# Performance work log

Hardware: AMD Instinct MI355X
Metric: run time of the kernel (lower is better)

Reference implementation:

```python
import jax, jax.numpy as jnp
import numpy as np

EMB = 1024
HEAD = 64

def setup_inputs() -> dict:
    key = jax.random.key(0)
    ks = jax.random.split(key, 7)
    s = 1.0 / np.sqrt(EMB)
    X = jax.random.normal(ks[0], (4, 4096, EMB), dtype=jnp.float32)
    Wk = jax.random.uniform(ks[1], (EMB, HEAD), jnp.float32, -s, s)
    bk = jax.random.uniform(ks[2], (HEAD,), jnp.float32, -s, s)
    Wq = jax.random.uniform(ks[3], (EMB, HEAD), jnp.float32, -s, s)
    bq = jax.random.uniform(ks[4], (HEAD,), jnp.float32, -s, s)
    Wv = jax.random.uniform(ks[5], (EMB, HEAD), jnp.float32, -s, s)
    bv = jax.random.uniform(ks[6], (HEAD,), jnp.float32, -s, s)
    return {"X": X, "Wk": Wk, "bk": bk, "Wq": Wq, "bq": bq, "Wv": Wv, "bv": bv}

def reference(X, Wk, bk, Wq, bq, Wv, bv):
    # X: [B, S, E]; projections -> [B, S, H]
    k = X @ Wk + bk
    q = X @ Wq + bq
    v = X @ Wv + bv
    S = X.shape[1]
    scale = 1.0 / np.sqrt(HEAD).astype(np.float32)
    scores = jnp.einsum('bqh,bkh->bqk', q, k) * scale  # [B, S, S]
    causal = jnp.tril(jnp.ones((S, S), dtype=bool))
    scores = jnp.where(causal, scores, -jnp.inf)
    probs = jax.nn.softmax(scores, axis=-1)
    return jnp.einsum('bqk,bkh->bqh', probs, v)
```

## Files before the change

### kernel.cpp

```cpp
#include <hip/hip_runtime.h>

#define S_LEN 4096
#define EMBD  1024
#define HEADD 64

typedef __bf16 bf16x8 __attribute__((ext_vector_type(8)));
typedef float  f32x4  __attribute__((ext_vector_type(4)));

__device__ __forceinline__ unsigned short f2bf(float f) {
  union { float f; unsigned u; } x; x.f = f;
  unsigned r = x.u + 0x7FFFu + ((x.u >> 16) & 1u);
  return (unsigned short)(r >> 16);
}

__device__ __forceinline__ bf16x8 cvt8(f32x4 a, f32x4 b) {
  union { bf16x8 v; unsigned short s[8]; } u;
#pragma unroll
  for (int j = 0; j < 4; j++) { u.s[j] = f2bf(a[j]); u.s[4 + j] = f2bf(b[j]); }
  return u.v;
}

__device__ __forceinline__ unsigned fbits(float f) {
  union { float f; unsigned u; } x; x.f = f; return x.u;
}

__global__ void prep_w(const float* __restrict__ Wk, const float* __restrict__ bk,
                       const float* __restrict__ Wq, const float* __restrict__ bq,
                       const float* __restrict__ Wv, const float* __restrict__ bv,
                       unsigned short* __restrict__ wt, float* __restrict__ bias) {
  int n = blockIdx.x;
  int t = threadIdx.x;
  const float QSCALE = 0.125f * 1.44269504088896340736f;
  const float* W; const float* bsrc; int col; float s = 1.0f;
  if (n < 64)       { W = Wk; bsrc = bk; col = n; }
  else if (n < 128) { W = Wq; bsrc = bq; col = n - 64; s = QSCALE; }
  else              { W = Wv; bsrc = bv; col = n - 128; }
  for (int k = t; k < EMBD; k += 256)
    wt[n * EMBD + k] = f2bf(W[k * HEADD + col] * s);
  if (t == 0) bias[n] = bsrc[col] * s;
}

__global__ __launch_bounds__(256, 1) void proj_qkv(
    const float* __restrict__ X, const unsigned short* __restrict__ wt,
    const float* __restrict__ bias,
    unsigned short* __restrict__ qws, unsigned short* __restrict__ kws,
    unsigned short* __restrict__ vtws) {
  __shared__ unsigned short xs[64 * 256];

  const int tid = threadIdx.x;
  const int w = tid >> 6;
  const int lane = tid & 63;
  const int l15 = lane & 15, lg = lane >> 4;
  const int row0 = blockIdx.x * 64;

  const int sr = tid >> 5;
  const int sc = (tid & 31) * 8;

  const unsigned short* wp = wt + (size_t)(w * 48 + l15) * EMBD + lg * 8;

  f32x4 acc[4][3];
#pragma unroll
  for (int g = 0; g < 4; g++)
#pragma unroll
    for (int j = 0; j < 3; j++) acc[g][j] = (f32x4){0.f, 0.f, 0.f, 0.f};

  f32x4 la[8], lb[8];
#pragma unroll
  for (int it = 0; it < 8; it++) {
    const float* src = X + (size_t)(row0 + it * 8 + sr) * EMBD + sc;
    la[it] = *(const f32x4*)src;
    lb[it] = *(const f32x4*)(src + 4);
  }
#pragma unroll
  for (int it = 0; it < 8; it++) {
    const int r = it * 8 + sr;
    int soff = (r << 8) + sc;
    soff ^= (r & 7) << 3;
    *(bf16x8*)&xs[soff] = cvt8(la[it], lb[it]);
  }
  __syncthreads();

#pragma unroll
  for (int kc = 0; kc < 4; kc++) {
    if (kc + 1 < 4) {
#pragma unroll
      for (int it = 0; it < 8; it++) {
        const float* src = X + (size_t)(row0 + it * 8 + sr) * EMBD + (kc + 1) * 256 + sc;
        la[it] = *(const f32x4*)src;
        lb[it] = *(const f32x4*)(src + 4);
      }
    }
    bf16x8 wf[2][3];
#pragma unroll
    for (int j = 0; j < 3; j++)
      wf[0][j] = *(const bf16x8*)(wp + (size_t)j * 16 * EMBD + kc * 256);
#pragma unroll
    for (int ss = 0; ss < 8; ss++) {
      const int cur = ss & 1;
      if (ss + 1 < 8) {
#pragma unroll
        for (int j = 0; j < 3; j++)
          wf[cur ^ 1][j] = *(const bf16x8*)(wp + (size_t)j * 16 * EMBD + kc * 256 + (ss + 1) * 32);
      }
      const int c = ss * 32 + lg * 8;
      bf16x8 a[4];
#pragma unroll
      for (int g = 0; g < 4; g++) {
        int so = ((g * 16 + l15) << 8) + c;
        so ^= (l15 & 7) << 3;
        a[g] = *(const bf16x8*)&xs[so];
      }
#pragma unroll
      for (int j = 0; j < 3; j++)
#pragma unroll
        for (int g = 0; g < 4; g++)
          acc[g][j] = __builtin_amdgcn_mfma_f32_16x16x32_bf16(a[g], wf[cur][j], acc[g][j], 0, 0, 0);
    }
    __syncthreads();
    if (kc + 1 < 4) {
#pragma unroll
      for (int it = 0; it < 8; it++) {
        const int r = it * 8 + sr;
        int soff = (r << 8) + sc;
        soff ^= (r & 7) << 3;
        *(bf16x8*)&xs[soff] = cvt8(la[it], lb[it]);
      }
      __syncthreads();
    }
  }

#pragma unroll
  for (int g = 0; g < 4; g++) {
    const int crow0 = row0 + g * 16 + lg * 4;
#pragma unroll
    for (int j = 0; j < 3; j++) {
      const int nf = w * 3 + j;
      const int n = nf * 16 + l15;
      const float bs = bias[n];
      if (nf < 8) {
        unsigned short* dst = (nf < 4) ? kws : qws;
        const int nn = n & 63;
#pragma unroll
        for (int i = 0; i < 4; i++)
          dst[(size_t)(crow0 + i) * HEADD + nn] = f2bf(acc[g][j][i] + bs);
      } else {
        const int d = n - 128;
        const int bb = crow0 >> 12, sr2 = crow0 & 4095;
        union { unsigned long long pk; unsigned short s[4]; } u;
#pragma unroll
        for (int i = 0; i < 4; i++) u.s[i] = f2bf(acc[g][j][i] + bs);
        *(unsigned long long*)&vtws[((size_t)bb * HEADD + d) * S_LEN + sr2] = u.pk;
      }
    }
  }
}

__global__ __launch_bounds__(512, 2) void attn(
    const unsigned short* __restrict__ qws,
    const unsigned short* __restrict__ kws,
    const unsigned short* __restrict__ vtws,
    unsigned short* __restrict__ pO,
    float* __restrict__ pmv, float* __restrict__ plv) {
  __shared__ uint4 kvb[2][1024];
  __shared__ unsigned short pbl[8][16][72];

  const int tid = threadIdx.x;
  const int w = tid >> 6;
  const int lane = tid & 63;
  const int l15 = lane & 15, lg = lane >> 4;
  const int srow = tid >> 3;
  const int scol = (tid & 7) * 8;
  const int soff = ((srow * 128 + (tid & 7) * 16)) ^ ((srow & 7) << 4);

  const int id = blockIdx.x;
  const int b = id & 3;
  const int x = (id >> 2) & 15;
  const int h = id >> 6;

  const unsigned short* kb = kws + (size_t)b * S_LEN * HEADD;
  const unsigned short* vb = vtws + (size_t)b * HEADD * S_LEN;
  const unsigned short* qp = qws + (size_t)b * S_LEN * HEADD;

  const int PH = 31 - x, PL = x;
  const int tlPH = 2 * PH + 1;
  const int tlwH = 2 * PH + (w >> 2);
  const int tlwL = 2 * PL + (w >> 2);
  const int qbH = PH * 128 + w * 16;
  const int qbL = PL * 128 + w * 16;

  const unsigned short* qH = qp + (size_t)(qbH + l15) * HEADD + lg * 8;
  const unsigned short* qL = qp + (size_t)(qbL + l15) * HEADD + lg * 8;
  const bf16x8 bqH0 = *(const bf16x8*)qH, bqH1 = *(const bf16x8*)(qH + 32);
  const bf16x8 bqL0 = *(const bf16x8*)qL, bqL1 = *(const bf16x8*)(qL + 32);

  f32x4 oH[4], oL[4];
#pragma unroll
  for (int nd = 0; nd < 4; nd++) {
    oH[nd] = (f32x4){0.f, 0.f, 0.f, 0.f};
    oL[nd] = (f32x4){0.f, 0.f, 0.f, 0.f};
  }
  float mH = -3.0e38f, lH = 0.f, mL = -3.0e38f, lL = 0.f;

#define PROC(BQ0, BQ1, O, M, LL, QB, TLX, tt, base)                             \
  do {                                                                          \
    bf16x8 k0[4], k1[4], v0[4], v1[4];                                          \
    _Pragma("unroll")                                                           \
    for (int nf = 0; nf < 4; nf++) {                                            \
      const int r = nf * 16 + l15;                                              \
      const int sw = (l15 & 7) << 4;                                            \
      const int b0 = (r * 128 + lg * 16) ^ sw;                                  \
      const int b1 = (r * 128 + 64 + lg * 16) ^ sw;                             \
      k0[nf] = *(const bf16x8*)&base[b0];                                       \
      k1[nf] = *(const bf16x8*)&base[b1];                                       \
      v0[nf] = *(const bf16x8*)&base[8192 + b0];                                \
      v1[nf] = *(const bf16x8*)&base[8192 + b1];                                \
    }                                                                           \
    f32x4 sc[4];                                                                \
    __builtin_amdgcn_s_setprio(1);                                              \
    _Pragma("unroll")                                                           \
    for (int nf = 0; nf < 4; nf++) {                                            \
      f32x4 z = (f32x4){0.f, 0.f, 0.f, 0.f};                                    \
      z = __builtin_amdgcn_mfma_f32_16x16x32_bf16(k0[nf], BQ0, z, 0, 0, 0);     \
      sc[nf] = __builtin_amdgcn_mfma_f32_16x16x32_bf16(k1[nf], BQ1, z, 0, 0, 0);\
    }                                                                           \
    __builtin_amdgcn_s_setprio(0);                                              \
    if ((tt) == (TLX)) {                                                        \
      const int qa = (QB) + l15;                                                \
      _Pragma("unroll")                                                         \
      for (int nf = 0; nf < 4; nf++)                                            \
        _Pragma("unroll")                                                       \
        for (int i = 0; i < 4; i++)                                             \
          if ((tt) * 64 + nf * 16 + lg * 4 + i > qa) sc[nf][i] = -1.0e30f;      \
    }                                                                           \
    float pm = sc[0][0];                                                        \
    _Pragma("unroll")                                                           \
    for (int nf = 0; nf < 4; nf++)                                              \
      _Pragma("unroll")                                                         \
      for (int i = 0; i < 4; i++) pm = fmaxf(pm, sc[nf][i]);                    \
    if (!__all(pm <= M + 8.0f)) {                                               \
      float mx = fmaxf(pm, __shfl_xor(pm, 16));                                 \
      mx = fmaxf(mx, __shfl_xor(mx, 32));                                       \
      const float mn = fmaxf(M, mx);                                            \
      const float al = __builtin_amdgcn_exp2f(M - mn);                          \
      M = mn;                                                                   \
      LL *= al;                                                                 \
      float alr[4];                                                             \
      _Pragma("unroll")                                                         \
      for (int i = 0; i < 4; i++) alr[i] = __shfl(al, lg * 4 + i);              \
      _Pragma("unroll")                                                         \
      for (int nd = 0; nd < 4; nd++)                                            \
        _Pragma("unroll")                                                       \
        for (int i = 0; i < 4; i++) O[nd][i] *= alr[i];                         \
    }                                                                           \
    _Pragma("unroll")                                                           \
    for (int nf = 0; nf < 4; nf++) {                                            \
      f32x4 p;                                                                  \
      _Pragma("unroll")                                                         \
      for (int i = 0; i < 4; i++) p[i] = __builtin_amdgcn_exp2f(sc[nf][i] - M); \
      LL += p[0] + p[1] + p[2] + p[3];                                          \
      unsigned lo_ = __builtin_amdgcn_perm(fbits(p[1]) + 0x8000u,               \
                                           fbits(p[0]) + 0x8000u, 0x07060302u); \
      unsigned hi_ = __builtin_amdgcn_perm(fbits(p[3]) + 0x8000u,               \
                                           fbits(p[2]) + 0x8000u, 0x07060302u); \
      uint2 pk_; pk_.x = lo_; pk_.y = hi_;                                      \
      *(uint2*)&pbl[w][l15][nf * 16 + lg * 4] = pk_;                            \
    }                                                                           \
    const bf16x8 ap0 = *(const bf16x8*)&pbl[w][l15][lg * 8];                    \
    const bf16x8 ap1 = *(const bf16x8*)&pbl[w][l15][32 + lg * 8];               \
    __builtin_amdgcn_s_setprio(1);                                              \
    _Pragma("unroll")                                                           \
    for (int nd = 0; nd < 4; nd++) {                                            \
      f32x4 oo = __builtin_amdgcn_mfma_f32_16x16x32_bf16(ap0, v0[nd], O[nd], 0, 0, 0); \
      O[nd] = __builtin_amdgcn_mfma_f32_16x16x32_bf16(ap1, v1[nd], oo, 0, 0, 0);\
    }                                                                           \
    __builtin_amdgcn_s_setprio(0);                                              \
  } while (0)

#define LOADG(tt)                                                               \
  do {                                                                          \
    kreg = *(const uint4*)(kb + ((size_t)(tt) * 64 + srow) * HEADD + scol);     \
    vreg = *(const uint4*)(vb + (size_t)srow * S_LEN + (tt) * 64 + scol);       \
  } while (0)

#define WRITEL(bf)                                                              \
  do {                                                                          \
    unsigned char* d_ = (unsigned char*)kvb[bf];                                \
    *(uint4*)&d_[soff] = kreg;                                                  \
    *(uint4*)&d_[8192 + soff] = vreg;                                           \
  } while (0)

  {
    uint4 kreg, vreg;
    int t = h;
    LOADG(t);
    WRITEL(0);
    __syncthreads();
    int cur = 0;
#pragma unroll 1
    while (true) {
      const int tn = t + 8;
      const bool hn = tn <= tlPH;
      if (hn) LOADG(tn);
      {
        const unsigned char* base = (const unsigned char*)kvb[cur];
        if (t <= tlwH) PROC(bqH0, bqH1, oH, mH, lH, qbH, tlwH, t, base);
        if (t <= tlwL) PROC(bqL0, bqL1, oL, mL, lL, qbL, tlwL, t, base);
      }
      if (!hn) break;
      WRITEL(cur ^ 1);
      __syncthreads();
      cur ^= 1;
      t = tn;
    }
  }

  lH += __shfl_xor(lH, 16);
  lH += __shfl_xor(lH, 32);
  lL += __shfl_xor(lL, 16);
  lL += __shfl_xor(lL, 32);
  const size_t pbH = (size_t)(h * 4 + b) * S_LEN + qbH;
  const size_t pbL = (size_t)(h * 4 + b) * S_LEN + qbL;
  if (lane < 16) {
    pmv[pbH + lane] = mH; plv[pbH + lane] = lH;
    pmv[pbL + lane] = mL; plv[pbL + lane] = lL;
  }
#pragma unroll
  for (int nd = 0; nd < 4; nd++)
#pragma unroll
    for (int i = 0; i < 4; i++) {
      pO[(pbH + lg * 4 + i) * 64 + nd * 16 + l15] = f2bf(oH[nd][i]);
      pO[(pbL + lg * 4 + i) * 64 + nd * 16 + l15] = f2bf(oL[nd][i]);
    }
#undef PROC
#undef LOADG
#undef WRITEL
}

__global__ __launch_bounds__(256) void merge_attn(
    const unsigned short* __restrict__ pO,
    const float* __restrict__ pmv, const float* __restrict__ plv,
    float* __restrict__ out) {
  const int row = blockIdx.x * 64 + (threadIdx.x >> 2);
  const int q = threadIdx.x & 3;
  float mh[8], lh[8];
  float M = -3.0e38f;
#pragma unroll
  for (int hh = 0; hh < 8; hh++) {
    mh[hh] = pmv[hh * 16384 + row];
    lh[hh] = plv[hh * 16384 + row];
    M = fmaxf(M, mh[hh]);
  }
  float Lt = 0.f, a[8];
#pragma unroll
  for (int hh = 0; hh < 8; hh++) {
    a[hh] = __builtin_amdgcn_exp2f(mh[hh] - M);
    Lt += a[hh] * lh[hh];
  }
  const float iL = 1.0f / Lt;
  float acc[16];
#pragma unroll
  for (int c = 0; c < 16; c++) acc[c] = 0.f;
#pragma unroll
  for (int hh = 0; hh < 8; hh++) {
    const unsigned short* src = pO + ((size_t)hh * 16384 + row) * 64 + q * 16;
    const uint4 u0 = *(const uint4*)(src);
    const uint4 u1 = *(const uint4*)(src + 8);
    const unsigned* uu0 = (const unsigned*)&u0;
    const unsigned* uu1 = (const unsigned*)&u1;
#pragma unroll
    for (int j = 0; j < 4; j++) {
      union { unsigned u; float f; } e0, e1, e2, e3;
      e0.u = uu0[j] << 16;  e1.u = uu0[j] & 0xffff0000u;
      e2.u = uu1[j] << 16;  e3.u = uu1[j] & 0xffff0000u;
      acc[j * 2 + 0] += e0.f * a[hh];
      acc[j * 2 + 1] += e1.f * a[hh];
      acc[8 + j * 2 + 0] += e2.f * a[hh];
      acc[8 + j * 2 + 1] += e3.f * a[hh];
    }
  }
  float* dst = out + (size_t)row * 64 + q * 16;
#pragma unroll
  for (int c = 0; c < 16; c++) dst[c] = acc[c] * iL;
}

extern "C" void kernel_launch(void* const* d_in, const int* in_sizes, int n_in,
                              void* d_out, int out_size, void* d_ws, size_t ws_size,
                              hipStream_t stream) {
  const float* X  = (const float*)d_in[0];
  const float* Wk = (const float*)d_in[1];
  const float* bk = (const float*)d_in[2];
  const float* Wq = (const float*)d_in[3];
  const float* bq = (const float*)d_in[4];
  const float* Wv = (const float*)d_in[5];
  const float* bv = (const float*)d_in[6];
  float* out = (float*)d_out;

  char* ws = (char*)d_ws;
  unsigned short* kws  = (unsigned short*)(ws);
  unsigned short* qws  = (unsigned short*)(ws + (2u << 20));
  unsigned short* vtws = (unsigned short*)(ws + (4u << 20));
  unsigned short* wt   = (unsigned short*)(ws + (6u << 20));
  float*          bias = (float*)(ws + (6u << 20) + (512u << 10));
  unsigned short* pO   = (unsigned short*)(ws + (8u << 20));
  float*          pmv  = (float*)(ws + (24u << 20));
  float*          plv  = (float*)(ws + (25u << 20));

  prep_w<<<dim3(192), dim3(256), 0, stream>>>(Wk, bk, Wq, bq, Wv, bv, wt, bias);
  proj_qkv<<<dim3(256), dim3(256), 0, stream>>>(X, wt, bias, qws, kws, vtws);
  attn<<<dim3(512), dim3(512), 0, stream>>>(qws, kws, vtws, pO, pmv, plv);
  merge_attn<<<dim3(256), dim3(256), 0, stream>>>(pO, pmv, plv, out);
}
```

Baseline: 65.63 us.

## Stream X tiles into double-buffered LDS via global_load_lds in QKV projection

The QKV projection kernel no longer loads fp32 X into registers, converts to bf16 and writes to LDS. It now issues direct global-to-LDS loads of raw fp32 data into a double-buffered 128KB shared array with an XOR swizzle. The bf16 conversion moves to the MFMA operand read path. This removes the register staging and one barrier per chunk so the next chunk's loads can overlap compute. The costs are doubled LDS footprint (fp32 instead of bf16, two buffers), extra conversion work repeated by each wave per fragment, and reliance on the async LDS load completing before the single barrier.

```diff
diff --git a/kernel.cpp b/kernel.cpp
--- a/kernel.cpp
+++ b/kernel.cpp
@@ -45,7 +45,7 @@
     const float* __restrict__ bias,
     unsigned short* __restrict__ qws, unsigned short* __restrict__ kws,
     unsigned short* __restrict__ vtws) {
-  __shared__ unsigned short xs[64 * 256];
+  __shared__ char xs[2][64 * 1024];
 
   const int tid = threadIdx.x;
   const int w = tid >> 6;
@@ -53,9 +53,6 @@
   const int l15 = lane & 15, lg = lane >> 4;
   const int row0 = blockIdx.x * 64;
 
-  const int sr = tid >> 5;
-  const int sc = (tid & 31) * 8;
-
   const unsigned short* wp = wt + (size_t)(w * 48 + l15) * EMBD + lg * 8;
 
   f32x4 acc[4][3];
@@ -64,70 +61,59 @@
 #pragma unroll
     for (int j = 0; j < 3; j++) acc[g][j] = (f32x4){0.f, 0.f, 0.f, 0.f};
 
-  f32x4 la[8], lb[8];
-#pragma unroll
-  for (int it = 0; it < 8; it++) {
-    const float* src = X + (size_t)(row0 + it * 8 + sr) * EMBD + sc;
-    la[it] = *(const f32x4*)src;
-    lb[it] = *(const f32x4*)(src + 4);
-  }
-#pragma unroll
-  for (int it = 0; it < 8; it++) {
-    const int r = it * 8 + sr;
-    int soff = (r << 8) + sc;
-    soff ^= (r & 7) << 3;
-    *(bf16x8*)&xs[soff] = cvt8(la[it], lb[it]);
-  }
+#define STAGE(bf, kc)                                                           \
+  do {                                                                          \
+    _Pragma("unroll")                                                           \
+    for (int it = 0; it < 16; it++) {                                           \
+      const int r = w * 16 + it;                                                \
+      const char* gp = (const char*)X + (((size_t)(row0 + r)) << 12)            \
+                       + (size_t)(kc)*1024 + ((lane * 16) ^ ((r & 7) << 4));    \
+      __builtin_amdgcn_global_load_lds(                                         \
+          (const __attribute__((address_space(1))) unsigned*)gp,                \
+          (__attribute__((address_space(3))) unsigned*)&xs[bf][r * 1024],       \
+          16, 0, 0);                                                            \
+    }                                                                           \
+  } while (0)
+
+  STAGE(0, 0);
   __syncthreads();
 
+  int cur = 0;
 #pragma unroll
   for (int kc = 0; kc < 4; kc++) {
-    if (kc + 1 < 4) {
-#pragma unroll
-      for (int it = 0; it < 8; it++) {
-        const float* src = X + (size_t)(row0 + it * 8 + sr) * EMBD + (kc + 1) * 256 + sc;
-        la[it] = *(const f32x4*)src;
-        lb[it] = *(const f32x4*)(src + 4);
-      }
-    }
+    if (kc + 1 < 4) STAGE(cur ^ 1, kc + 1);
     bf16x8 wf[2][3];
 #pragma unroll
     for (int j = 0; j < 3; j++)
       wf[0][j] = *(const bf16x8*)(wp + (size_t)j * 16 * EMBD + kc * 256);
 #pragma unroll
     for (int ss = 0; ss < 8; ss++) {
-      const int cur = ss & 1;
+      const int pp = ss & 1;
       if (ss + 1 < 8) {
 #pragma unroll
         for (int j = 0; j < 3; j++)
-          wf[cur ^ 1][j] = *(const bf16x8*)(wp + (size_t)j * 16 * EMBD + kc * 256 + (ss + 1) * 32);
+          wf[pp ^ 1][j] = *(const bf16x8*)(wp + (size_t)j * 16 * EMBD + kc * 256 + (ss + 1) * 32);
       }
-      const int c = ss * 32 + lg * 8;
+      const int cb = ss * 128 + lg * 32;
       bf16x8 a[4];
 #pragma unroll
       for (int g = 0; g < 4; g++) {
-        int so = ((g * 16 + l15) << 8) + c;
-        so ^= (l15 & 7) << 3;
-        a[g] = *(const bf16x8*)&xs[so];
+        const int r = g * 16 + l15;
+        const int swz = (r & 7) << 4;
+        const f32x4 u0 = *(const f32x4*)&xs[cur][r * 1024 + (cb ^ swz)];
+        const f32x4 u1 = *(const f32x4*)&xs[cur][r * 1024 + ((cb + 16) ^ swz)];
+        a[g] = cvt8(u0, u1);
       }
 #pragma unroll
       for (int j = 0; j < 3; j++)
 #pragma unroll
         for (int g = 0; g < 4; g++)
-          acc[g][j] = __builtin_amdgcn_mfma_f32_16x16x32_bf16(a[g], wf[cur][j], acc[g][j], 0, 0, 0);
+          acc[g][j] = __builtin_amdgcn_mfma_f32_16x16x32_bf16(a[g], wf[pp][j], acc[g][j], 0, 0, 0);
     }
     __syncthreads();
-    if (kc + 1 < 4) {
-#pragma unroll
-      for (int it = 0; it < 8; it++) {
-        const int r = it * 8 + sr;
-        int soff = (r << 8) + sc;
-        soff ^= (r & 7) << 3;
-        *(bf16x8*)&xs[soff] = cvt8(la[it], lb[it]);
-      }
-      __syncthreads();
-    }
-  }
+    cur ^= 1;
+  }
+#undef STAGE
 
 #pragma unroll
   for (int g = 0; g < 4; g++) {
```

Result: slower. 68.51 us (+4.4%).
